# Performance work log

Measured on AMD Instinct MI355X. Metric: run time of the kernel, lower is better.

## Reference

```python
import jax, jax.numpy as jnp
import numpy as np
import math

VOCAB = 32000
D = 2048
H = 16
KVH = 4
HD = D // H          # 128
FF = 5632
L = 2
S = 2048
B = 1
EPS = 1e-5
ROPE_BASE = 10000.0


def setup_inputs() -> dict:
    key = jax.random.key(0)
    ks = jax.random.split(key, 12)
    sc = 0.02
    # RoPE table: [S, HD//2, 2] (cos, sin), matching precompute_freqs_cis
    inv = 1.0 / (ROPE_BASE ** (jnp.arange(0, HD, 2, dtype=jnp.float32) / HD))
    pos = jnp.arange(S, dtype=jnp.float32)
    f = jnp.outer(pos, inv)
    freqs_cis = jnp.stack([jnp.cos(f), jnp.sin(f)], axis=-1)
    mask = jnp.tril(jnp.ones((S, S), dtype=bool))
    return {
        "input_ids": jax.random.randint(ks[0], (B, S), 0, VOCAB, dtype=jnp.int32),
        "mask": mask,
        "freqs_cis": freqs_cis,
        "w_embed": jax.random.normal(ks[1], (VOCAB, D), jnp.float32) * sc,
        "wqkv": jax.random.normal(ks[2], (L, D, D + 2 * KVH * HD), jnp.float32) * sc,
        "wo": jax.random.normal(ks[3], (L, D, D), jnp.float32) * sc,
        "w1": jax.random.normal(ks[4], (L, D, FF), jnp.float32) * sc,
        "w3": jax.random.normal(ks[5], (L, D, FF), jnp.float32) * sc,
        "w2": jax.random.normal(ks[6], (L, FF, D), jnp.float32) * sc,
        "attn_norm_w": jnp.ones((L, D), jnp.float32),
        "ff_norm_w": jnp.ones((L, D), jnp.float32),
        "final_norm_w": jnp.ones((D,), jnp.float32),
        "w_head": jax.random.normal(ks[7], (D, VOCAB), jnp.float32) * sc,
    }


def _rmsnorm(x, w):
    xf = x.astype(jnp.float32)
    n = xf * jax.lax.rsqrt(jnp.mean(xf * xf, axis=-1, keepdims=True) + EPS)
    return n.astype(x.dtype) * w


def _rope(x, fc):
    # x: [b, h, s, hd]; fc: [s, hd/2, 2]
    xr = x.reshape(*x.shape[:-1], HD // 2, 2)
    cos, sin = fc[..., 0], fc[..., 1]  # [s, hd/2] broadcast over b,h
    out = jnp.stack([xr[..., 0] * cos - xr[..., 1] * sin,
                     xr[..., 1] * cos + xr[..., 0] * sin], axis=-1)
    return out.reshape(x.shape).astype(x.dtype)


def _attention(x, mask, fc, wqkv, wo):
    b, s, _ = x.shape
    qkv = x @ wqkv  # [b, s, D + 2*kv_dim]
    kv_dim = KVH * HD
    q, k, v = jnp.split(qkv, [D, D + kv_dim], axis=-1)
    q = q.reshape(b, s, H, HD).transpose(0, 2, 1, 3)      # [b,H,s,hd]
    k = k.reshape(b, s, KVH, HD).transpose(0, 2, 1, 3)    # [b,KVH,s,hd]
    v = v.reshape(b, s, KVH, HD).transpose(0, 2, 1, 3)
    q = _rope(q, fc)
    k = _rope(k, fc)
    rep = H // KVH
    k = jnp.repeat(k, rep, axis=1)  # [b,H,s,hd]
    v = jnp.repeat(v, rep, axis=1)
    scores = jnp.einsum('bhqd,bhkd->bhqk', q, k) / math.sqrt(HD)
    scores = jnp.where(mask, scores, -1e30)
    attn = jax.nn.softmax(scores, axis=-1)
    out = jnp.einsum('bhqk,bhkd->bhqd', attn, v)
    out = out.transpose(0, 2, 1, 3).reshape(b, s, D)
    return out @ wo


def reference(input_ids, mask, freqs_cis, w_embed, wqkv, wo, w1, w3, w2,
              attn_norm_w, ff_norm_w, final_norm_w, w_head):
    x = w_embed[input_ids]  # [B,S,D]
    for l in range(L):
        h = x + _attention(_rmsnorm(x, attn_norm_w[l]), mask, freqs_cis,
                           wqkv[l], wo[l])
        hn = _rmsnorm(h, ff_norm_w[l])
        x = h + (jax.nn.silu(hn @ w1[l]) * (hn @ w3[l])) @ w2[l]
    x = _rmsnorm(x, final_norm_w)
    return x @ w_head  # [B,S,VOCAB]
```

## Files before the change

### kernel.cpp

```cpp
#include <hip/hip_runtime.h>

#define DD 2048
#define SEQ 2048
#define NH 16
#define NKV 4
#define HD 128
#define FFD 5632
#define NL 2

typedef __bf16 bf16x8 __attribute__((ext_vector_type(8)));
typedef float f32x4 __attribute__((ext_vector_type(4)));

#define AS1 __attribute__((address_space(1)))
#define AS3 __attribute__((address_space(3)))

__device__ __forceinline__ unsigned short f2bf(float f) {
    unsigned int u = __builtin_bit_cast(unsigned int, f);
    u += 0x7fffu + ((u >> 16) & 1u);
    return (unsigned short)(u >> 16);
}

__global__ __launch_bounds__(256)
void embed_gather(const int* __restrict__ ids, const float* __restrict__ wemb,
                  float* __restrict__ x)
{
    int s = blockIdx.x;
    int id = ids[s];
    const float4* src = (const float4*)(wemb + (size_t)id * DD);
    float4* dst = (float4*)(x + (size_t)s * DD);
    dst[threadIdx.x] = src[threadIdx.x];
    dst[threadIdx.x + 256] = src[threadIdx.x + 256];
}

__global__ __launch_bounds__(256)
void rmsnorm_bf16(const float* __restrict__ x, const float* __restrict__ w,
                  unsigned short* __restrict__ out)
{
    int row = blockIdx.x;
    int t = threadIdx.x;
    const float4* xr = (const float4*)(x + (size_t)row * DD);
    float4 v0 = xr[t], v1 = xr[t + 256];
    float ss = v0.x * v0.x + v0.y * v0.y + v0.z * v0.z + v0.w * v0.w
             + v1.x * v1.x + v1.y * v1.y + v1.z * v1.z + v1.w * v1.w;
#pragma unroll
    for (int off = 32; off; off >>= 1) ss += __shfl_down(ss, off);
    __shared__ float red[4];
    if ((t & 63) == 0) red[t >> 6] = ss;
    __syncthreads();
    float sc = rsqrtf((red[0] + red[1] + red[2] + red[3]) * (1.0f / DD) + 1e-5f);
    const float4* wr = (const float4*)w;
    float4 w0 = wr[t], w1v = wr[t + 256];
    ushort4 o0, o1;
    o0.x = f2bf(v0.x * sc * w0.x);  o0.y = f2bf(v0.y * sc * w0.y);
    o0.z = f2bf(v0.z * sc * w0.z);  o0.w = f2bf(v0.w * sc * w0.w);
    o1.x = f2bf(v1.x * sc * w1v.x); o1.y = f2bf(v1.y * sc * w1v.y);
    o1.z = f2bf(v1.z * sc * w1v.z); o1.w = f2bf(v1.w * sc * w1v.w);
    ushort4* op = (ushort4*)(out + (size_t)row * DD);
    op[t] = o0;
    op[t + 256] = o1;
}

__global__ __launch_bounds__(256)
void transpose_cast(const float* __restrict__ src, unsigned short* __restrict__ dst,
                    int ld_src, int ld_dst, size_t sb, size_t db)
{
    __shared__ float tile[64][65];
    src += (size_t)blockIdx.z * sb;
    dst += (size_t)blockIdx.z * db;
    int c0 = blockIdx.x * 64, r0 = blockIdx.y * 64;
    int tx = threadIdx.x & 15, ty = threadIdx.x >> 4;
#pragma unroll
    for (int i = 0; i < 4; ++i) {
        int r = ty + i * 16;
        float4 v = *(const float4*)(src + (size_t)(r0 + r) * ld_src + c0 + tx * 4);
        tile[r][tx * 4 + 0] = v.x; tile[r][tx * 4 + 1] = v.y;
        tile[r][tx * 4 + 2] = v.z; tile[r][tx * 4 + 3] = v.w;
    }
    __syncthreads();
#pragma unroll
    for (int i = 0; i < 4; ++i) {
        int c = ty + i * 16;
        ushort4 o;
        o.x = f2bf(tile[tx * 4 + 0][c]); o.y = f2bf(tile[tx * 4 + 1][c]);
        o.z = f2bf(tile[tx * 4 + 2][c]); o.w = f2bf(tile[tx * 4 + 3][c]);
        *(ushort4*)(dst + (size_t)(c0 + c) * ld_dst + r0 + tx * 4) = o;
    }
}

__global__ void rope_qk(const float* __restrict__ qkv, const float* __restrict__ fc,
                        unsigned short* __restrict__ Qb, unsigned short* __restrict__ Kb)
{
    int s = blockIdx.x;
    int hh = blockIdx.y;
    int i = threadIdx.x;
    float2 cs = *(const float2*)(fc + ((size_t)s * 64 + i) * 2);
    const float* src;
    unsigned short* dst;
    if (hh < NH) {
        src = qkv + (size_t)s * 3072 + hh * HD;
        dst = Qb + ((size_t)hh * SEQ + s) * HD;
    } else {
        int kh = hh - NH;
        src = qkv + (size_t)s * 3072 + DD + kh * HD;
        dst = Kb + ((size_t)kh * SEQ + s) * HD;
    }
    float2 xv = *(const float2*)(src + 2 * i);
    ushort2 o;
    o.x = f2bf(xv.x * cs.x - xv.y * cs.y);
    o.y = f2bf(xv.y * cs.x + xv.x * cs.y);
    *(ushort2*)(dst + 2 * i) = o;
}

__global__ __launch_bounds__(256)
void silu_mul(const float* __restrict__ h, unsigned short* __restrict__ g)
{
    size_t i = (size_t)blockIdx.x * 256 + threadIdx.x;
    size_t row = i / (FFD / 4), c4 = i % (FFD / 4);
    const float* p = h + row * (2 * FFD) + c4 * 4;
    float4 a = *(const float4*)(p);
    float4 b = *(const float4*)(p + FFD);
    ushort4 o;
    o.x = f2bf(a.x / (1.f + __expf(-a.x)) * b.x);
    o.y = f2bf(a.y / (1.f + __expf(-a.y)) * b.y);
    o.z = f2bf(a.z / (1.f + __expf(-a.z)) * b.z);
    o.w = f2bf(a.w / (1.f + __expf(-a.w)) * b.w);
    *(ushort4*)(g + row * FFD + c4 * 4) = o;
}

__global__ __launch_bounds__(256)
void gemm_bf16(const unsigned short* __restrict__ A, const unsigned short* __restrict__ B,
               float* __restrict__ C, const float* __restrict__ Res,
               int N, int K, int mT)
{
    __shared__ __attribute__((aligned(16))) unsigned char smem[65536];
    const int tid = threadIdx.x;
    const int lane = tid & 63;
    const int w = tid >> 6;
    const int nwg = gridDim.x;
    const int qq = nwg >> 3;
    const int logical = ((int)blockIdx.x & 7) * qq + ((int)blockIdx.x >> 3);
    const int m0 = (logical % mT) * 128;
    const int n0 = (logical / mT) * 128;
    const int wm = (w >> 1) * 64, wn = (w & 1) * 64;
    const int lrow = lane & 15, lgrp = lane >> 4;
    const int NT = K >> 6;

    f32x4 acc[4][4];
#pragma unroll
    for (int i = 0; i < 4; ++i)
#pragma unroll
        for (int j = 0; j < 4; ++j) acc[i][j] = 0.f;

    auto stage = [&](int bsel, int kt) {
#pragma unroll
        for (int it = 0; it < 4; ++it) {
            int o = it * 4096 + tid * 16;
            int row = o >> 7;
            int col = (o & 127) ^ ((row & 7) << 4);
            const char* ga = (const char*)A + ((size_t)(m0 + row) * K + kt) * 2 + col;
            const char* gb = (const char*)B + ((size_t)(n0 + row) * K + kt) * 2 + col;
            __builtin_amdgcn_global_load_lds(
                (AS1 const void*)ga,
                (AS3 void*)(smem + bsel * 32768 + it * 4096 + w * 1024),
                16, 0, 0);
            __builtin_amdgcn_global_load_lds(
                (AS1 const void*)gb,
                (AS3 void*)(smem + bsel * 32768 + 16384 + it * 4096 + w * 1024),
                16, 0, 0);
        }
    };

    stage(0, 0);
    int cur = 0;
    for (int t = 0; t < NT; ++t) {
        if (t + 1 < NT) {
            stage(cur ^ 1, (t + 1) << 6);
            asm volatile("s_waitcnt vmcnt(8)" ::: "memory");
        } else {
            asm volatile("s_waitcnt vmcnt(0)" ::: "memory");
        }
        __builtin_amdgcn_s_barrier();
        __builtin_amdgcn_sched_barrier(0);
        const unsigned char* buf = smem + cur * 32768;
#pragma unroll
        for (int kk = 0; kk < 2; ++kk) {
            bf16x8 af[4], bfr[4];
            int cb = kk * 64 + lgrp * 16;
#pragma unroll
            for (int i = 0; i < 4; ++i) {
                int ra = wm + i * 16 + lrow;
                af[i] = *(const bf16x8*)(buf + ra * 128 + (cb ^ ((ra & 7) << 4)));
                int rb = wn + i * 16 + lrow;
                bfr[i] = *(const bf16x8*)(buf + 16384 + rb * 128 + (cb ^ ((rb & 7) << 4)));
            }
#pragma unroll
            for (int i = 0; i < 4; ++i)
#pragma unroll
                for (int j = 0; j < 4; ++j)
                    acc[i][j] = __builtin_amdgcn_mfma_f32_16x16x32_bf16(af[i], bfr[j], acc[i][j], 0, 0, 0);
        }
        __builtin_amdgcn_s_barrier();
        cur ^= 1;
    }

    const bool hasRes = (Res != nullptr);
#pragma unroll
    for (int i = 0; i < 4; ++i)
#pragma unroll
        for (int j = 0; j < 4; ++j) {
            int r = m0 + wm + i * 16 + lgrp * 4;
            int c = n0 + wn + j * 16 + lrow;
#pragma unroll
            for (int jj = 0; jj < 4; ++jj) {
                size_t idx = (size_t)(r + jj) * N + c;
                float v = acc[i][j][jj];
                if (hasRes) v += Res[idx];
                C[idx] = v;
            }
        }
}

__global__ __launch_bounds__(512, 1)
void gemm_bf16_256(const unsigned short* __restrict__ A, const unsigned short* __restrict__ B,
                   float* __restrict__ C, int N, int K, int mT)
{
    __shared__ __attribute__((aligned(16))) unsigned char smem[131072];
    const int tid = threadIdx.x;
    const int lane = tid & 63;
    const int w = tid >> 6;
    const int nwg = gridDim.x;
    const int qq = nwg >> 3;
    const int logical = ((int)blockIdx.x & 7) * qq + ((int)blockIdx.x >> 3);
    const int m0 = (logical % mT) * 256;
    const int n0 = (logical / mT) * 256;
    const int wm2 = (w >> 2) * 128;
    const int lrow = lane & 15, lgrp = (lane >> 4) & 3;
    const int NT = K >> 5;

    f32x4 acc[8][4];
#pragma unroll
    for (int i = 0; i < 8; ++i)
#pragma unroll
        for (int j = 0; j < 4; ++j) acc[i][j] = 0.f;

    const int X = (((lrow & 1) << 6) | (lgrp << 4)) ^ ((lrow >> 1) << 4);
    const int aoff = ((wm2 >> 1) + (lrow >> 1)) * 128 + X;
    const int boff = 16384 + (((w & 3) * 32) + (lrow >> 1)) * 128 + X;

    auto stage_part = [&](int ktile, int part) {
        const unsigned short* base = part ? B : A;
        const int r0 = part ? n0 : m0;
        const int ktb = ktile << 6;
#pragma unroll
        for (int j = 0; j < 2; ++j) {
            int o = j * 8192 + tid * 16;
            int p = o >> 7;
            int sl = (o & 127) ^ ((p & 7) << 4);
            int r = 2 * p + (sl >> 6);
            int cb = sl & 63;
            const char* g = (const char*)base + (size_t)(r0 + r) * K * 2 + ktb + cb;
            __builtin_amdgcn_global_load_lds(
                (AS1 const void*)g,
                (AS3 void*)(smem + (ktile & 3) * 32768 + part * 16384 + o),
                16, 0, 0);
        }
    };

#pragma unroll
    for (int p0 = 0; p0 < 3; ++p0) { stage_part(p0, 0); stage_part(p0, 1); }

    for (int t = 0; t < NT; ++t) {
        const unsigned char* buf = smem + (t & 3) * 32768;
        const bool have3 = (t + 3 < NT);
        if (have3) stage_part(t + 3, 0);
        if (have3)              asm volatile("s_waitcnt vmcnt(10)" ::: "memory");
        else if (t + 2 < NT)    asm volatile("s_waitcnt vmcnt(8)"  ::: "memory");
        else if (t + 1 < NT)    asm volatile("s_waitcnt vmcnt(4)"  ::: "memory");
        else                    asm volatile("s_waitcnt vmcnt(0)"  ::: "memory");
        __builtin_amdgcn_s_barrier();
        __builtin_amdgcn_sched_barrier(0);
        bf16x8 bfr[4], afr[4];
#pragma unroll
        for (int nj = 0; nj < 4; ++nj) bfr[nj] = *(const bf16x8*)(buf + boff + nj * 1024);
#pragma unroll
        for (int mi = 0; mi < 4; ++mi) afr[mi] = *(const bf16x8*)(buf + aoff + mi * 1024);
        __builtin_amdgcn_s_setprio(1);
#pragma unroll
        for (int mi = 0; mi < 4; ++mi)
#pragma unroll
            for (int nj = 0; nj < 4; ++nj)
                acc[mi][nj] = __builtin_amdgcn_mfma_f32_16x16x32_bf16(afr[mi], bfr[nj], acc[mi][nj], 0, 0, 0);
        __builtin_amdgcn_s_setprio(0);
        bf16x8 afr2[4];
#pragma unroll
        for (int mi = 0; mi < 4; ++mi) afr2[mi] = *(const bf16x8*)(buf + aoff + (mi + 4) * 1024);
        if (have3) stage_part(t + 3, 1);
        asm volatile("s_waitcnt lgkmcnt(0)" ::: "memory");
        __builtin_amdgcn_sched_barrier(0);
        __builtin_amdgcn_s_barrier();
        __builtin_amdgcn_sched_barrier(0);
        __builtin_amdgcn_s_setprio(1);
#pragma unroll
        for (int mi = 0; mi < 4; ++mi)
#pragma unroll
            for (int nj = 0; nj < 4; ++nj)
                acc[mi + 4][nj] = __builtin_amdgcn_mfma_f32_16x16x32_bf16(afr2[mi], bfr[nj], acc[mi + 4][nj], 0, 0, 0);
        __builtin_amdgcn_s_setprio(0);
    }

#pragma unroll
    for (int mi = 0; mi < 8; ++mi)
#pragma unroll
        for (int nj = 0; nj < 4; ++nj) {
            int r = m0 + wm2 + mi * 16 + lgrp * 4;
            int c = n0 + (w & 3) * 64 + nj * 16 + lrow;
#pragma unroll
            for (int jj = 0; jj < 4; ++jj)
                C[(size_t)(r + jj) * N + c] = acc[mi][nj][jj];
        }
}

__global__ __launch_bounds__(256)
void attn_fwd(const unsigned short* __restrict__ Qb, const unsigned short* __restrict__ Kb,
              const unsigned short* __restrict__ VTb, unsigned short* __restrict__ O)
{
    __shared__ __attribute__((aligned(16))) unsigned char smem[73728];
    const int qb = 31 - (int)blockIdx.x;
    const int h = blockIdx.y;
    const int kvh = h >> 2;
    const int tid = threadIdx.x, lane = tid & 63, w = tid >> 6;
    const int lrow = lane & 15, lgrp = lane >> 4;
    const int q0 = qb * 64 + w * 16;

    bf16x8 qf[4];
    const unsigned short* qrow = Qb + ((size_t)h * SEQ + q0 + lrow) * HD;
#pragma unroll
    for (int c = 0; c < 4; ++c)
        qf[c] = *(const bf16x8*)(qrow + c * 32 + lgrp * 8);

    float m[4], l[4];
    f32x4 oacc[8];
#pragma unroll
    for (int j = 0; j < 8; ++j) oacc[j] = 0.f;
#pragma unroll
    for (int j = 0; j < 4; ++j) { m[j] = -3.0e38f; l[j] = 0.f; }

    const float scale = 0.08838834764831845f;
    const char* kbase = (const char*)(Kb + (size_t)kvh * SEQ * HD);
    const char* vbase = (const char*)(VTb + (size_t)kvh * HD * SEQ);
    unsigned char* Pl = smem + 65536 + w * 2048;

    auto stage_kv = [&](int bsel, int t) {
#pragma unroll
        for (int it = 0; it < 4; ++it) {
            int o = it * 4096 + tid * 16;
            int row = o >> 8, col = o & 255;
            int scol = col ^ ((row & 7) << 4);
            const char* g = kbase + (size_t)(t * 64 + row) * 256 + scol;
            __builtin_amdgcn_global_load_lds(
                (AS1 const void*)g,
                (AS3 void*)(smem + bsel * 32768 + it * 4096 + w * 1024),
                16, 0, 0);
        }
#pragma unroll
        for (int it = 0; it < 4; ++it) {
            int o = it * 4096 + tid * 16;
            int row = o >> 7, col = o & 127;
            int scol = col ^ ((row & 7) << 4);
            const char* g = vbase + (size_t)row * (SEQ * 2) + (size_t)t * 128 + scol;
            __builtin_amdgcn_global_load_lds(
                (AS1 const void*)g,
                (AS3 void*)(smem + bsel * 32768 + 16384 + it * 4096 + w * 1024),
                16, 0, 0);
        }
    };

    stage_kv(0, 0);
    int cur = 0;
    for (int t = 0; t <= qb; ++t) {
        if (t < qb) {
            stage_kv(cur ^ 1, t + 1);
            asm volatile("s_waitcnt vmcnt(8)" ::: "memory");
        } else {
            asm volatile("s_waitcnt vmcnt(0)" ::: "memory");
        }
        __builtin_amdgcn_s_barrier();
        __builtin_amdgcn_sched_barrier(0);
        const unsigned char* kb = smem + cur * 32768;
        const unsigned char* vtb = kb + 16384;

        f32x4 sf[4];
#pragma unroll
        for (int kf = 0; kf < 4; ++kf) sf[kf] = 0.f;
#pragma unroll
        for (int kf = 0; kf < 4; ++kf) {
            int rb = kf * 16 + lrow;
            int rbase = rb * 256;
            int sw = (rb & 7) << 4;
#pragma unroll
            for (int c = 0; c < 4; ++c) {
                bf16x8 kfr = *(const bf16x8*)(kb + rbase + ((c * 64 + lgrp * 16) ^ sw));
                sf[kf] = __builtin_amdgcn_mfma_f32_16x16x32_bf16(qf[c], kfr, sf[kf], 0, 0, 0);
            }
        }
        const bool diag = (t == qb);
        float mx[4] = {-3.0e38f, -3.0e38f, -3.0e38f, -3.0e38f};
#pragma unroll
        for (int kf = 0; kf < 4; ++kf)
#pragma unroll
            for (int j = 0; j < 4; ++j) {
                float v = sf[kf][j] * scale;
                if (diag && (t * 64 + kf * 16 + lrow) > (q0 + lgrp * 4 + j)) v = -3.0e38f;
                sf[kf][j] = v;
                mx[j] = fmaxf(mx[j], v);
            }
#pragma unroll
        for (int off = 1; off < 16; off <<= 1)
#pragma unroll
            for (int j = 0; j < 4; ++j) mx[j] = fmaxf(mx[j], __shfl_xor(mx[j], off));
        float alpha[4], rs[4];
#pragma unroll
        for (int j = 0; j < 4; ++j) {
            float mn = fmaxf(m[j], mx[j]);
            alpha[j] = __expf(m[j] - mn);
            m[j] = mn;
            rs[j] = 0.f;
        }
#pragma unroll
        for (int kf = 0; kf < 4; ++kf)
#pragma unroll
            for (int j = 0; j < 4; ++j) {
                float p = __expf(sf[kf][j] - m[j]);
                rs[j] += p;
                int qq = lgrp * 4 + j;
                int addr = qq * 128 + (((kf * 16 + lrow) * 2) ^ ((qq & 7) << 4));
                *(unsigned short*)(Pl + addr) = f2bf(p);
            }
#pragma unroll
        for (int off = 1; off < 16; off <<= 1)
#pragma unroll
            for (int j = 0; j < 4; ++j) rs[j] += __shfl_xor(rs[j], off);
#pragma unroll
        for (int j = 0; j < 4; ++j) l[j] = l[j] * alpha[j] + rs[j];
#pragma unroll
        for (int hf = 0; hf < 8; ++hf)
#pragma unroll
            for (int j = 0; j < 4; ++j) oacc[hf][j] *= alpha[j];
#pragma unroll
        for (int c = 0; c < 2; ++c) {
            int cb = c * 64 + lgrp * 16;
            bf16x8 pf = *(const bf16x8*)(Pl + lrow * 128 + (cb ^ ((lrow & 7) << 4)));
#pragma unroll
            for (int hf = 0; hf < 8; ++hf) {
                int rv = hf * 16 + lrow;
                bf16x8 vf = *(const bf16x8*)(vtb + rv * 128 + (cb ^ ((rv & 7) << 4)));
                oacc[hf] = __builtin_amdgcn_mfma_f32_16x16x32_bf16(pf, vf, oacc[hf], 0, 0, 0);
            }
        }
        __builtin_amdgcn_s_barrier();
        cur ^= 1;
    }
#pragma unroll
    for (int hf = 0; hf < 8; ++hf)
#pragma unroll
        for (int j = 0; j < 4; ++j) {
            float v = oacc[hf][j] / l[j];
            int qg = q0 + lgrp * 4 + j;
            O[(size_t)qg * DD + h * HD + hf * 16 + lrow] = f2bf(v);
        }
}

extern "C" void kernel_launch(void* const* d_in, const int* in_sizes, int n_in,
                              void* d_out, int out_size, void* d_ws, size_t ws_size,
                              hipStream_t stream)
{
    (void)in_sizes; (void)n_in; (void)out_size; (void)ws_size;
    const int* ids = (const int*)d_in[0];
    const float* fc   = (const float*)d_in[2];
    const float* wemb = (const float*)d_in[3];
    const float* wqkv = (const float*)d_in[4];
    const float* wo   = (const float*)d_in[5];
    const float* w1   = (const float*)d_in[6];
    const float* w3   = (const float*)d_in[7];
    const float* w2   = (const float*)d_in[8];
    const float* anw  = (const float*)d_in[9];
    const float* fnw  = (const float*)d_in[10];
    const float* finw = (const float*)d_in[11];
    const float* wh   = (const float*)d_in[12];
    float* out = (float*)d_out;
    char* ws = (char*)d_ws;

    unsigned short* WQKVT = (unsigned short*)(ws);
    unsigned short* WOT   = (unsigned short*)(ws + 25165824);
    unsigned short* W13T  = (unsigned short*)(ws + 41943040);
    unsigned short* W2T   = (unsigned short*)(ws + 134217728);
    unsigned short* WHT   = (unsigned short*)(ws + 180355072);
    float*          X     = (float*)(ws + 311427072);
    unsigned short* XN    = (unsigned short*)(ws + 328204288);
    float*          QKV   = (float*)(ws + 336592896);
    unsigned short* Qb    = (unsigned short*)(ws + 361758720);
    unsigned short* Kb    = (unsigned short*)(ws + 370147328);
    unsigned short* VT    = (unsigned short*)(ws + 372244480);
    unsigned short* AO    = (unsigned short*)(ws + 374341632);
    float*          H13   = (float*)(ws + 382730240);
    unsigned short* G     = (unsigned short*)(ws + 475004928);

    transpose_cast<<<dim3(48, 32, 2), 256, 0, stream>>>(wqkv, WQKVT, 3072, 2048,
        (size_t)2048 * 3072, (size_t)3072 * 2048);
    transpose_cast<<<dim3(32, 32, 2), 256, 0, stream>>>(wo, WOT, 2048, 2048,
        (size_t)2048 * 2048, (size_t)2048 * 2048);
    transpose_cast<<<dim3(88, 32, 2), 256, 0, stream>>>(w1, W13T, 5632, 2048,
        (size_t)2048 * 5632, (size_t)11264 * 2048);
    transpose_cast<<<dim3(88, 32, 2), 256, 0, stream>>>(w3, W13T + (size_t)5632 * 2048, 5632, 2048,
        (size_t)2048 * 5632, (size_t)11264 * 2048);
    transpose_cast<<<dim3(32, 88, 2), 256, 0, stream>>>(w2, W2T, 2048, 5632,
        (size_t)5632 * 2048, (size_t)2048 * 5632);
    transpose_cast<<<dim3(500, 32, 1), 256, 0, stream>>>(wh, WHT, 32000, 2048, 0, 0);

    embed_gather<<<dim3(SEQ), 256, 0, stream>>>(ids, wemb, X);

    for (int lyr = 0; lyr < NL; ++lyr) {
        const unsigned short* wqkvT_l = WQKVT + (size_t)lyr * 3072 * 2048;
        const unsigned short* woT_l   = WOT   + (size_t)lyr * 2048 * 2048;
        const unsigned short* w13T_l  = W13T  + (size_t)lyr * 11264 * 2048;
        const unsigned short* w2T_l   = W2T   + (size_t)lyr * 2048 * 5632;

        rmsnorm_bf16<<<dim3(SEQ), 256, 0, stream>>>(X, anw + lyr * DD, XN);
        gemm_bf16<<<dim3(24 * 16), 256, 0, stream>>>(XN, wqkvT_l, QKV, nullptr, 3072, 2048, 16);
        rope_qk<<<dim3(SEQ, NH + NKV), 64, 0, stream>>>(QKV, fc, Qb, Kb);
        transpose_cast<<<dim3(2, 32, 4), 256, 0, stream>>>(QKV + 2560, VT, 3072, 2048,
            128, (size_t)128 * 2048);
        attn_fwd<<<dim3(32, NH), 256, 0, stream>>>(Qb, Kb, VT, AO);
        gemm_bf16<<<dim3(16 * 16), 256, 0, stream>>>(AO, woT_l, X, X, 2048, 2048, 16);
        rmsnorm_bf16<<<dim3(SEQ), 256, 0, stream>>>(X, fnw + lyr * DD, XN);
        gemm_bf16_256<<<dim3(8 * 44), 512, 0, stream>>>(XN, w13T_l, H13, 11264, 2048, 8);
        silu_mul<<<dim3(11264), 256, 0, stream>>>(H13, G);
        gemm_bf16<<<dim3(16 * 16), 256, 0, stream>>>(G, w2T_l, X, X, 2048, 5632, 16);
    }
    rmsnorm_bf16<<<dim3(SEQ), 256, 0, stream>>>(X, finw, XN);
    gemm_bf16_256<<<dim3(8 * 125), 512, 0, stream>>>(XN, WHT, out, 32000, 2048, 8);
}
```

Measured before the change: 1.276 ms.

## Fuse SiLU-gate into W1/W3 GEMM epilogue and software-pipeline LDS fragment reads

Interleaves W1 and W3 rows in 16-row groups during the weight transpose so each wave's accumulator tile holds matching h1/h3 columns. The 256-tile GEMM epilogue can then compute silu(h1)*h3 and write bf16 G directly. This removes the fp32 H13 intermediate round-trip and the separate silu_mul launch. The GEMM main loop is also restructured to double-buffer register fragments, prefetching the next tile's LDS reads before the second MFMA half with finer waitcnt control. The risk is more register pressure and subtler synchronisation.

New measurement: 1.214 ms. -4.8%, faster.

```diff
diff --git a/kernel.cpp b/kernel.cpp
--- a/kernel.cpp
+++ b/kernel.cpp
@@ -62,7 +62,7 @@
 
 __global__ __launch_bounds__(256)
 void transpose_cast(const float* __restrict__ src, unsigned short* __restrict__ dst,
-                    int ld_src, int ld_dst, size_t sb, size_t db)
+                    int ld_src, int ld_dst, size_t sb, size_t db, int nmap)
 {
     __shared__ float tile[64][65];
     src += (size_t)blockIdx.z * sb;
@@ -80,10 +80,14 @@
 #pragma unroll
     for (int i = 0; i < 4; ++i) {
         int c = ty + i * 16;
+        int cc = c0 + c;
+        int dr = cc;
+        if (nmap == 1) dr = ((cc >> 4) << 5) | (cc & 15);
+        else if (nmap == 2) dr = (((cc >> 4) << 5) | (cc & 15)) + 16;
         ushort4 o;
         o.x = f2bf(tile[tx * 4 + 0][c]); o.y = f2bf(tile[tx * 4 + 1][c]);
         o.z = f2bf(tile[tx * 4 + 2][c]); o.w = f2bf(tile[tx * 4 + 3][c]);
-        *(ushort4*)(dst + (size_t)(c0 + c) * ld_dst + r0 + tx * 4) = o;
+        *(ushort4*)(dst + (size_t)dr * ld_dst + r0 + tx * 4) = o;
     }
 }
 
@@ -109,22 +113,6 @@
     o.x = f2bf(xv.x * cs.x - xv.y * cs.y);
     o.y = f2bf(xv.y * cs.x + xv.x * cs.y);
     *(ushort2*)(dst + 2 * i) = o;
-}
-
-__global__ __launch_bounds__(256)
-void silu_mul(const float* __restrict__ h, unsigned short* __restrict__ g)
-{
-    size_t i = (size_t)blockIdx.x * 256 + threadIdx.x;
-    size_t row = i / (FFD / 4), c4 = i % (FFD / 4);
-    const float* p = h + row * (2 * FFD) + c4 * 4;
-    float4 a = *(const float4*)(p);
-    float4 b = *(const float4*)(p + FFD);
-    ushort4 o;
-    o.x = f2bf(a.x / (1.f + __expf(-a.x)) * b.x);
-    o.y = f2bf(a.y / (1.f + __expf(-a.y)) * b.y);
-    o.z = f2bf(a.z / (1.f + __expf(-a.z)) * b.z);
-    o.w = f2bf(a.w / (1.f + __expf(-a.w)) * b.w);
-    *(ushort4*)(g + row * FFD + c4 * 4) = o;
 }
 
 __global__ __launch_bounds__(256)
@@ -220,9 +208,10 @@
         }
 }
 
+template<int FUSE>
 __global__ __launch_bounds__(512, 1)
 void gemm_bf16_256(const unsigned short* __restrict__ A, const unsigned short* __restrict__ B,
-                   float* __restrict__ C, int N, int K, int mT)
+                   void* __restrict__ Cout, int N, int K, int mT)
 {
     __shared__ __attribute__((aligned(16))) unsigned char smem[131072];
     const int tid = threadIdx.x;
@@ -266,58 +255,94 @@
         }
     };
 
-#pragma unroll
-    for (int p0 = 0; p0 < 3; ++p0) { stage_part(p0, 0); stage_part(p0, 1); }
-
-    for (int t = 0; t < NT; ++t) {
+    bf16x8 bE[4], aE[4], bO[4], aO[4], a47[4];
+
+    auto read_ba = [&](int t, bf16x8* bs, bf16x8* as) {
         const unsigned char* buf = smem + (t & 3) * 32768;
-        const bool have3 = (t + 3 < NT);
-        if (have3) stage_part(t + 3, 0);
-        if (have3)              asm volatile("s_waitcnt vmcnt(10)" ::: "memory");
-        else if (t + 2 < NT)    asm volatile("s_waitcnt vmcnt(8)"  ::: "memory");
-        else if (t + 1 < NT)    asm volatile("s_waitcnt vmcnt(4)"  ::: "memory");
-        else                    asm volatile("s_waitcnt vmcnt(0)"  ::: "memory");
-        __builtin_amdgcn_s_barrier();
-        __builtin_amdgcn_sched_barrier(0);
-        bf16x8 bfr[4], afr[4];
-#pragma unroll
-        for (int nj = 0; nj < 4; ++nj) bfr[nj] = *(const bf16x8*)(buf + boff + nj * 1024);
-#pragma unroll
-        for (int mi = 0; mi < 4; ++mi) afr[mi] = *(const bf16x8*)(buf + aoff + mi * 1024);
-        __builtin_amdgcn_s_setprio(1);
-#pragma unroll
-        for (int mi = 0; mi < 4; ++mi)
-#pragma unroll
-            for (int nj = 0; nj < 4; ++nj)
-                acc[mi][nj] = __builtin_amdgcn_mfma_f32_16x16x32_bf16(afr[mi], bfr[nj], acc[mi][nj], 0, 0, 0);
-        __builtin_amdgcn_s_setprio(0);
-        bf16x8 afr2[4];
-#pragma unroll
-        for (int mi = 0; mi < 4; ++mi) afr2[mi] = *(const bf16x8*)(buf + aoff + (mi + 4) * 1024);
-        if (have3) stage_part(t + 3, 1);
-        asm volatile("s_waitcnt lgkmcnt(0)" ::: "memory");
-        __builtin_amdgcn_sched_barrier(0);
-        __builtin_amdgcn_s_barrier();
+#pragma unroll
+        for (int nj = 0; nj < 4; ++nj) bs[nj] = *(const bf16x8*)(buf + boff + nj * 1024);
+#pragma unroll
+        for (int mi = 0; mi < 4; ++mi) as[mi] = *(const bf16x8*)(buf + aoff + mi * 1024);
+    };
+
+    auto tile = [&](int t, bf16x8* bc, bf16x8* ac, bf16x8* bn, bf16x8* an) {
+        const unsigned char* buf = smem + (t & 3) * 32768;
+        if (t + 3 < NT) stage_part(t + 3, 0);
+#pragma unroll
+        for (int mi = 0; mi < 4; ++mi) a47[mi] = *(const bf16x8*)(buf + aoff + (mi + 4) * 1024);
+        asm volatile("s_waitcnt lgkmcnt(4)" ::: "memory");
         __builtin_amdgcn_sched_barrier(0);
         __builtin_amdgcn_s_setprio(1);
 #pragma unroll
         for (int mi = 0; mi < 4; ++mi)
 #pragma unroll
             for (int nj = 0; nj < 4; ++nj)
-                acc[mi + 4][nj] = __builtin_amdgcn_mfma_f32_16x16x32_bf16(afr2[mi], bfr[nj], acc[mi + 4][nj], 0, 0, 0);
+                acc[mi][nj] = __builtin_amdgcn_mfma_f32_16x16x32_bf16(ac[mi], bc[nj], acc[mi][nj], 0, 0, 0);
         __builtin_amdgcn_s_setprio(0);
-    }
-
-#pragma unroll
-    for (int mi = 0; mi < 8; ++mi)
-#pragma unroll
-        for (int nj = 0; nj < 4; ++nj) {
-            int r = m0 + wm2 + mi * 16 + lgrp * 4;
-            int c = n0 + (w & 3) * 64 + nj * 16 + lrow;
-#pragma unroll
-            for (int jj = 0; jj < 4; ++jj)
-                C[(size_t)(r + jj) * N + c] = acc[mi][nj][jj];
-        }
+        if (t + 3 < NT) stage_part(t + 3, 1);
+        if (t + 1 < NT) {
+            if (t + 3 < NT)      { asm volatile("s_waitcnt vmcnt(8)" ::: "memory"); }
+            else if (t + 2 < NT) { asm volatile("s_waitcnt vmcnt(4)" ::: "memory"); }
+            else                 { asm volatile("s_waitcnt vmcnt(0)" ::: "memory"); }
+            __builtin_amdgcn_s_barrier();
+            __builtin_amdgcn_sched_barrier(0);
+            read_ba(t + 1, bn, an);
+            asm volatile("s_waitcnt lgkmcnt(8)" ::: "memory");
+        } else {
+            asm volatile("s_waitcnt lgkmcnt(0)" ::: "memory");
+        }
+        __builtin_amdgcn_sched_barrier(0);
+        __builtin_amdgcn_s_setprio(1);
+#pragma unroll
+        for (int mi = 0; mi < 4; ++mi)
+#pragma unroll
+            for (int nj = 0; nj < 4; ++nj)
+                acc[mi + 4][nj] = __builtin_amdgcn_mfma_f32_16x16x32_bf16(a47[mi], bc[nj], acc[mi + 4][nj], 0, 0, 0);
+        __builtin_amdgcn_s_setprio(0);
+    };
+
+#pragma unroll
+    for (int p0 = 0; p0 < 3; ++p0) { stage_part(p0, 0); stage_part(p0, 1); }
+    asm volatile("s_waitcnt vmcnt(8)" ::: "memory");
+    __builtin_amdgcn_s_barrier();
+    __builtin_amdgcn_sched_barrier(0);
+    read_ba(0, bE, aE);
+
+    for (int tt = 0; tt < NT; tt += 2) {
+        tile(tt, bE, aE, bO, aO);
+        tile(tt + 1, bO, aO, bE, aE);
+    }
+
+    if constexpr (FUSE == 0) {
+        float* C = (float*)Cout;
+#pragma unroll
+        for (int mi = 0; mi < 8; ++mi)
+#pragma unroll
+            for (int nj = 0; nj < 4; ++nj) {
+                int r = m0 + wm2 + mi * 16 + lgrp * 4;
+                int c = n0 + (w & 3) * 64 + nj * 16 + lrow;
+#pragma unroll
+                for (int jj = 0; jj < 4; ++jj)
+                    C[(size_t)(r + jj) * N + c] = acc[mi][nj][jj];
+            }
+    } else {
+        unsigned short* G = (unsigned short*)Cout;
+        const int nbase = n0 + (w & 3) * 64;
+#pragma unroll
+        for (int mi = 0; mi < 8; ++mi)
+#pragma unroll
+            for (int p = 0; p < 2; ++p) {
+                int r = m0 + wm2 + mi * 16 + lgrp * 4;
+                int cc = (nbase >> 1) + p * 16 + lrow;
+#pragma unroll
+                for (int jj = 0; jj < 4; ++jj) {
+                    float h1 = acc[mi][2 * p][jj];
+                    float h3 = acc[mi][2 * p + 1][jj];
+                    float g = h1 / (1.f + __expf(-h1)) * h3;
+                    G[(size_t)(r + jj) * FFD + cc] = f2bf(g);
+                }
+            }
+    }
 }
 
 __global__ __launch_bounds__(256)
@@ -502,20 +527,19 @@
     unsigned short* Kb    = (unsigned short*)(ws + 370147328);
     unsigned short* VT    = (unsigned short*)(ws + 372244480);
     unsigned short* AO    = (unsigned short*)(ws + 374341632);
-    float*          H13   = (float*)(ws + 382730240);
     unsigned short* G     = (unsigned short*)(ws + 475004928);
 
     transpose_cast<<<dim3(48, 32, 2), 256, 0, stream>>>(wqkv, WQKVT, 3072, 2048,
-        (size_t)2048 * 3072, (size_t)3072 * 2048);
+        (size_t)2048 * 3072, (size_t)3072 * 2048, 0);
     transpose_cast<<<dim3(32, 32, 2), 256, 0, stream>>>(wo, WOT, 2048, 2048,
-        (size_t)2048 * 2048, (size_t)2048 * 2048);
+        (size_t)2048 * 2048, (size_t)2048 * 2048, 0);
     transpose_cast<<<dim3(88, 32, 2), 256, 0, stream>>>(w1, W13T, 5632, 2048,
-        (size_t)2048 * 5632, (size_t)11264 * 2048);
-    transpose_cast<<<dim3(88, 32, 2), 256, 0, stream>>>(w3, W13T + (size_t)5632 * 2048, 5632, 2048,
-        (size_t)2048 * 5632, (size_t)11264 * 2048);
+        (size_t)2048 * 5632, (size_t)11264 * 2048, 1);
+    transpose_cast<<<dim3(88, 32, 2), 256, 0, stream>>>(w3, W13T, 5632, 2048,
+        (size_t)2048 * 5632, (size_t)11264 * 2048, 2);
     transpose_cast<<<dim3(32, 88, 2), 256, 0, stream>>>(w2, W2T, 2048, 5632,
-        (size_t)5632 * 2048, (size_t)2048 * 5632);
-    transpose_cast<<<dim3(500, 32, 1), 256, 0, stream>>>(wh, WHT, 32000, 2048, 0, 0);
+        (size_t)5632 * 2048, (size_t)2048 * 5632, 0);
+    transpose_cast<<<dim3(500, 32, 1), 256, 0, stream>>>(wh, WHT, 32000, 2048, 0, 0, 0);
 
     embed_gather<<<dim3(SEQ), 256, 0, stream>>>(ids, wemb, X);
 
@@ -529,14 +553,13 @@
         gemm_bf16<<<dim3(24 * 16), 256, 0, stream>>>(XN, wqkvT_l, QKV, nullptr, 3072, 2048, 16);
         rope_qk<<<dim3(SEQ, NH + NKV), 64, 0, stream>>>(QKV, fc, Qb, Kb);
         transpose_cast<<<dim3(2, 32, 4), 256, 0, stream>>>(QKV + 2560, VT, 3072, 2048,
-            128, (size_t)128 * 2048);
+            128, (size_t)128 * 2048, 0);
         attn_fwd<<<dim3(32, NH), 256, 0, stream>>>(Qb, Kb, VT, AO);
         gemm_bf16<<<dim3(16 * 16), 256, 0, stream>>>(AO, woT_l, X, X, 2048, 2048, 16);
         rmsnorm_bf16<<<dim3(SEQ), 256, 0, stream>>>(X, fnw + lyr * DD, XN);
-        gemm_bf16_256<<<dim3(8 * 44), 512, 0, stream>>>(XN, w13T_l, H13, 11264, 2048, 8);
-        silu_mul<<<dim3(11264), 256, 0, stream>>>(H13, G);
+        gemm_bf16_256<1><<<dim3(8 * 44), 512, 0, stream>>>(XN, w13T_l, G, 11264, 2048, 8);
         gemm_bf16<<<dim3(16 * 16), 256, 0, stream>>>(G, w2T_l, X, X, 2048, 5632, 16);
     }
     rmsnorm_bf16<<<dim3(SEQ), 256, 0, stream>>>(X, finw, XN);
-    gemm_bf16_256<<<dim3(8 * 125), 512, 0, stream>>>(XN, WHT, out, 32000, 2048, 8);
-}
+    gemm_bf16_256<0><<<dim3(8 * 125), 512, 0, stream>>>(XN, WHT, out, 32000, 2048, 8);
+}
```
